# Kernel tuning notes

Hardware: AMD Instinct MI355X
Metric: run time of the kernel (lower is better)

## Reference

```python
import jax, jax.numpy as jnp
import numpy as np

H = 2048  # hidden_size == input_size
L = 2048  # max_length == seq_len


def setup_inputs() -> dict:
    key = jax.random.key(0)
    ks = jax.random.split(key, 5)
    bound = 1.0 / np.sqrt(H)  # torch nn.GRU default init: U(-1/sqrt(H), 1/sqrt(H))
    u = lambda k, shape: jax.random.uniform(k, shape, jnp.float32, -bound, bound)
    return {
        "x": jax.random.normal(ks[0], (L, H), jnp.float32),
        "w_ih": u(ks[1], (3 * H, H)),  # rows ordered [reset; update; new], torch layout
        "w_hh": u(ks[2], (3 * H, H)),
        "b_ih": u(ks[3], (3 * H,)),
        "b_hh": u(ks[4], (3 * H,)),
    }


def reference(x, w_ih, w_hh, b_ih, b_hh):
    # Faithful single-layer GRU (torch semantics), batch=1, hidden init to zeros.
    def step(h, x_t):
        gi = x_t @ w_ih.T + b_ih          # (3H,)
        gh = h @ w_hh.T + b_hh            # (3H,)
        i_r, i_z, i_n = jnp.split(gi, 3)
        h_r, h_z, h_n = jnp.split(gh, 3)
        r = jax.nn.sigmoid(i_r + h_r)
        z = jax.nn.sigmoid(i_z + h_z)
        n = jnp.tanh(i_n + r * h_n)
        h_new = (1.0 - z) * n + z * h
        return h_new, h_new

    h0 = jnp.zeros((H,), x.dtype)
    h_final, outputs = jax.lax.scan(step, h0, x)  # outputs: (L, H)
    hidden = h_final.reshape(1, 1, H)  # matches torch (num_layers, batch, H)
    return outputs, hidden, hidden
```

## Files before the change

kernel.cpp:

```cpp
#include <hip/hip_runtime.h>
#include <math.h>

#define HID 2048
#define SEQ 2048
#define N3  6144
#define NBLK 256
#define NREG 8

#define BM 128
#define BN 128
#define BK 16

__global__ __launch_bounds__(256)
void gi_gemm_kernel(const float* __restrict__ X, const float* __restrict__ W,
                    const float* __restrict__ bias, float* __restrict__ GI) {
  __shared__ float As[BK][BM + 4];
  __shared__ float Bs[BK][BN + 4];
  const int tid = threadIdx.x;
  const int bm = blockIdx.y * BM;
  const int bn = blockIdx.x * BN;
  const int tx = tid & 15;
  const int ty = tid >> 4;
  const int lr = tid >> 1;
  const int lk = (tid & 1) * 8;

  float acc[8][8];
#pragma unroll
  for (int i = 0; i < 8; ++i)
#pragma unroll
    for (int j = 0; j < 8; ++j) acc[i][j] = 0.f;

  const float* Arow = X + (size_t)(bm + lr) * HID + lk;
  const float* Brow = W + (size_t)(bn + lr) * HID + lk;

  for (int kc = 0; kc < HID; kc += BK) {
    float4 a0 = *(const float4*)(Arow + kc);
    float4 a1 = *(const float4*)(Arow + kc + 4);
    float4 b0 = *(const float4*)(Brow + kc);
    float4 b1 = *(const float4*)(Brow + kc + 4);
    __syncthreads();
    As[lk + 0][lr] = a0.x; As[lk + 1][lr] = a0.y; As[lk + 2][lr] = a0.z; As[lk + 3][lr] = a0.w;
    As[lk + 4][lr] = a1.x; As[lk + 5][lr] = a1.y; As[lk + 6][lr] = a1.z; As[lk + 7][lr] = a1.w;
    Bs[lk + 0][lr] = b0.x; Bs[lk + 1][lr] = b0.y; Bs[lk + 2][lr] = b0.z; Bs[lk + 3][lr] = b0.w;
    Bs[lk + 4][lr] = b1.x; Bs[lk + 5][lr] = b1.y; Bs[lk + 6][lr] = b1.z; Bs[lk + 7][lr] = b1.w;
    __syncthreads();
#pragma unroll
    for (int kk = 0; kk < BK; ++kk) {
      float4 av0 = *(const float4*)&As[kk][ty * 8];
      float4 av1 = *(const float4*)&As[kk][ty * 8 + 4];
      float4 bv0 = *(const float4*)&Bs[kk][tx * 8];
      float4 bv1 = *(const float4*)&Bs[kk][tx * 8 + 4];
      float a[8] = {av0.x, av0.y, av0.z, av0.w, av1.x, av1.y, av1.z, av1.w};
      float b[8] = {bv0.x, bv0.y, bv0.z, bv0.w, bv1.x, bv1.y, bv1.z, bv1.w};
#pragma unroll
      for (int i = 0; i < 8; ++i)
#pragma unroll
        for (int j = 0; j < 8; ++j)
          acc[i][j] = fmaf(a[i], b[j], acc[i][j]);
    }
  }

  const int n0 = bn + tx * 8;
  float bv[8];
#pragma unroll
  for (int j = 0; j < 8; ++j) bv[j] = bias[n0 + j];
#pragma unroll
  for (int i = 0; i < 8; ++i) {
    float4 o0, o1;
    o0.x = acc[i][0] + bv[0]; o0.y = acc[i][1] + bv[1];
    o0.z = acc[i][2] + bv[2]; o0.w = acc[i][3] + bv[3];
    o1.x = acc[i][4] + bv[4]; o1.y = acc[i][5] + bv[5];
    o1.z = acc[i][6] + bv[6]; o1.w = acc[i][7] + bv[7];
    float* Crow = GI + (size_t)(bm + ty * 8 + i) * N3 + n0;
    *(float4*)Crow = o0;
    *(float4*)(Crow + 4) = o1;
  }
}

template <int CTRL, int ROW_MASK>
__device__ __forceinline__ float dpp_add(float x) {
  int y = __builtin_amdgcn_update_dpp(0, __float_as_uint(x), CTRL, ROW_MASK, 0xf, true);
  return x + __uint_as_float(y);
}

__device__ __forceinline__ float wave_sum(float x) {
  x = dpp_add<0x111, 0xf>(x);
  x = dpp_add<0x112, 0xf>(x);
  x = dpp_add<0x114, 0xf>(x);
  x = dpp_add<0x118, 0xf>(x);
  x = dpp_add<0x142, 0xa>(x);
  x = dpp_add<0x143, 0xc>(x);
  return __uint_as_float(__builtin_amdgcn_readlane(__float_as_uint(x), 63));
}

__device__ __forceinline__ float rlane(float x, int l) {
  return __uint_as_float(__builtin_amdgcn_readlane(__float_as_uint(x), l));
}

__device__ __forceinline__ float sigf(float x) {
  return __builtin_amdgcn_rcpf(1.f + __expf(-x));
}
__device__ __forceinline__ float tanhfast(float x) {
  return 1.f - 2.f * __builtin_amdgcn_rcpf(1.f + __expf(2.f * x));
}

__device__ __forceinline__ float unpk24(unsigned u) {
  return __uint_as_float((u & 0x00FFFFFFu) << 8);
}

__device__ __forceinline__ void ld_quad2(const unsigned long long* pa,
                                         const unsigned long long* pb,
                                         uint4& qa, uint4& qb) {
  asm volatile("global_load_dwordx4 %0, %2, off sc1\n\t"
               "global_load_dwordx4 %1, %3, off sc1\n\t"
               "s_waitcnt vmcnt(0)"
               : "=&v"(qa), "=&v"(qb)
               : "v"(pa), "v"(pb)
               : "memory");
}

__global__ __launch_bounds__(256, 1)
void gru_recurrent_kernel(const float* __restrict__ Whh,
                          const float* __restrict__ bhh,
                          const float* __restrict__ GI,
                          float* __restrict__ out,
                          unsigned long long* hpk,
                          int t0, int t1) {
  __shared__ float lds_h[2][HID];
  const int tid  = threadIdx.x;
  const int lane = tid & 63;
  const int wv   = tid >> 6;
  const int gw   = blockIdx.x * 4 + wv;
  const int i0   = 2 * gw;
  const int reg  = blockIdx.x & (NREG - 1);

  const int rows[6] = {i0, i0 + 1, HID + i0, HID + i0 + 1, 2 * HID + i0, 2 * HID + i0 + 1};

  float4 w[6][8];
#pragma unroll
  for (int r = 0; r < 6; ++r) {
    const float* wr = Whh + (size_t)rows[r] * HID + lane * 4;
#pragma unroll
    for (int jb = 0; jb < 8; ++jb) {
      w[r][jb] = *(const float4*)(wr + jb * 256);
      asm volatile("" : "+a"(w[r][jb].x), "+a"(w[r][jb].y),
                        "+a"(w[r][jb].z), "+a"(w[r][jb].w));
    }
  }

  float br0, br1, bz0, bz1, bn0, bn1;
  {
    float a = 0.f, b = 0.f, c = 0.f;
    if (lane < 2) {
      a = bhh[i0 + lane];
      b = bhh[HID + i0 + lane];
      c = bhh[2 * HID + i0 + lane];
    }
    br0 = rlane(a, 0); br1 = rlane(a, 1);
    bz0 = rlane(b, 0); bz1 = rlane(b, 1);
    bn0 = rlane(c, 0); bn1 = rlane(c, 1);
  }

  float gr = 0.f, gz = 0.f, gn = 0.f;
  if (lane < 2) {
    gr = GI[i0 + lane];
    gz = GI[HID + i0 + lane];
    gn = GI[2 * HID + i0 + lane];
  }

  const int s0 = tid * 2;

  long long d_prev = 0;
  long long period = 0;
  const long long MARGIN = 1500;

  for (int t = t0; t < t1; ++t) {
    if (period > 0) {
      const long long target = d_prev + period - MARGIN;
      while ((long long)__builtin_amdgcn_s_memtime() < target)
        __builtin_amdgcn_s_sleep(1);
    }

    float pr = 0.f, pz = 0.f, pn = 0.f;
    if (t + 1 < t1 && lane < 2) {
      const float* g = GI + (size_t)(t + 1 - t0) * N3;
      pr = g[i0 + lane];
      pz = g[HID + i0 + lane];
      pn = g[2 * HID + i0 + lane];
    }
    asm volatile("" ::: "memory");

    const unsigned long long* hb = hpk + ((size_t)reg * 2 + (t & 1)) * (HID / 2);
    const unsigned long long* pa = hb + s0;
    const unsigned long long* pb = hb + 512 + s0;
    const unsigned tb = (unsigned)t & 0xFFu;
    uint4 qa, qb;
    ld_quad2(pa, pb, qa, qb);
    for (;;) {
      const bool ok = ((qa.x >> 24) == tb) & ((qa.y >> 24) == tb) &
                      ((qa.z >> 24) == tb) & ((qa.w >> 24) == tb) &
                      ((qb.x >> 24) == tb) & ((qb.y >> 24) == tb) &
                      ((qb.z >> 24) == tb) & ((qb.w >> 24) == tb);
      if (ok) break;
      ld_quad2(pa, pb, qa, qb);
    }

    {
      const long long now = (long long)__builtin_amdgcn_s_memtime();
      if (d_prev > 0) {
        const long long iv = now - d_prev;
        period = (period > 0) ? period + ((iv - period) >> 3) : iv;
        if (period > 20000) period = 20000;
        if (period < 0) period = 0;
      }
      d_prev = now;
    }

    float* lc = lds_h[t & 1];
    float4 v0, v1;
    v0.x = unpk24(qa.x); v0.y = unpk24(qa.y);
    v0.z = unpk24(qa.z); v0.w = unpk24(qa.w);
    v1.x = unpk24(qb.x); v1.y = unpk24(qb.y);
    v1.z = unpk24(qb.z); v1.w = unpk24(qb.w);
    *(float4*)&lc[tid * 4] = v0;
    *(float4*)&lc[1024 + tid * 4] = v1;
    __syncthreads();

    const float hp0 = lc[i0], hp1 = lc[i0 + 1];

    float4 hv[8];
    float acc0 = 0.f, acc1 = 0.f, acc2 = 0.f, acc3 = 0.f;
#pragma unroll
    for (int jb = 0; jb < 8; ++jb) {
      hv[jb] = *(const float4*)&lc[jb * 256 + lane * 4];
      acc0 = fmaf(w[0][jb].x, hv[jb].x, acc0); acc0 = fmaf(w[0][jb].y, hv[jb].y, acc0);
      acc0 = fmaf(w[0][jb].z, hv[jb].z, acc0); acc0 = fmaf(w[0][jb].w, hv[jb].w, acc0);
      acc1 = fmaf(w[1][jb].x, hv[jb].x, acc1); acc1 = fmaf(w[1][jb].y, hv[jb].y, acc1);
      acc1 = fmaf(w[1][jb].z, hv[jb].z, acc1); acc1 = fmaf(w[1][jb].w, hv[jb].w, acc1);
      acc2 = fmaf(w[2][jb].x, hv[jb].x, acc2); acc2 = fmaf(w[2][jb].y, hv[jb].y, acc2);
      acc2 = fmaf(w[2][jb].z, hv[jb].z, acc2); acc2 = fmaf(w[2][jb].w, hv[jb].w, acc2);
      acc3 = fmaf(w[3][jb].x, hv[jb].x, acc3); acc3 = fmaf(w[3][jb].y, hv[jb].y, acc3);
      acc3 = fmaf(w[3][jb].z, hv[jb].z, acc3); acc3 = fmaf(w[3][jb].w, hv[jb].w, acc3);
    }

    const float sr0 = wave_sum(acc0), sr1 = wave_sum(acc1);
    const float sz0 = wave_sum(acc2), sz1 = wave_sum(acc3);

    const float gr0 = rlane(gr, 0), gr1 = rlane(gr, 1);
    const float gz0 = rlane(gz, 0), gz1 = rlane(gz, 1);
    const float gn0 = rlane(gn, 0), gn1 = rlane(gn, 1);

    const float r0 = sigf(gr0 + sr0 + br0);
    const float r1 = sigf(gr1 + sr1 + br1);
    const float z0 = sigf(gz0 + sz0 + bz0);
    const float z1 = sigf(gz1 + sz1 + bz1);

    float acc4 = 0.f, acc5 = 0.f;
#pragma unroll
    for (int jb = 0; jb < 8; ++jb) {
      acc4 = fmaf(w[4][jb].x, hv[jb].x, acc4); acc4 = fmaf(w[4][jb].y, hv[jb].y, acc4);
      acc4 = fmaf(w[4][jb].z, hv[jb].z, acc4); acc4 = fmaf(w[4][jb].w, hv[jb].w, acc4);
      acc5 = fmaf(w[5][jb].x, hv[jb].x, acc5); acc5 = fmaf(w[5][jb].y, hv[jb].y, acc5);
      acc5 = fmaf(w[5][jb].z, hv[jb].z, acc5); acc5 = fmaf(w[5][jb].w, hv[jb].w, acc5);
    }
    const float sn0 = wave_sum(acc4), sn1 = wave_sum(acc5);

    const float n0 = tanhfast(gn0 + r0 * (sn0 + bn0));
    const float n1 = tanhfast(gn1 + r1 * (sn1 + bn1));
    const float hn0 = (1.f - z0) * n0 + z0 * hp0;
    const float hn1 = (1.f - z1) * n1 + z1 * hp1;

    {
      const unsigned nt = ((unsigned)(t + 1) & 0xFFu) << 24;
      const unsigned u0 = (__float_as_uint(hn0) + 0x80u) >> 8;
      const unsigned u1 = (__float_as_uint(hn1) + 0x80u) >> 8;
      const unsigned long long pk =
          ((unsigned long long)(nt | (u1 & 0x00FFFFFFu)) << 32) |
          (nt | (u0 & 0x00FFFFFFu));
      if (lane < NREG) {
        __hip_atomic_store(hpk + ((size_t)lane * 2 + ((t + 1) & 1)) * (HID / 2) + gw,
                           pk, __ATOMIC_RELAXED, __HIP_MEMORY_SCOPE_AGENT);
      }
    }

    if (t > 0 && (t & (NBLK - 1)) == blockIdx.x) {
      float* orow = out + (size_t)(t - 1) * HID;
      *(float4*)(orow + tid * 4) = v0;
      *(float4*)(orow + 1024 + tid * 4) = v1;
    }

    if (t == SEQ - 1 && lane == 0) {
      float2 hv2; hv2.x = hn0; hv2.y = hn1;
      *(float2*)(out + (size_t)t * HID + i0) = hv2;
      *(float2*)(out + (size_t)SEQ * HID + i0) = hv2;
      *(float2*)(out + (size_t)SEQ * HID + HID + i0) = hv2;
    }

    gr = pr; gz = pz; gn = pn;
  }
}

extern "C" void kernel_launch(void* const* d_in, const int* in_sizes, int n_in,
                              void* d_out, int out_size, void* d_ws, size_t ws_size,
                              hipStream_t stream) {
  const float* x    = (const float*)d_in[0];
  const float* w_ih = (const float*)d_in[1];
  const float* w_hh = (const float*)d_in[2];
  const float* b_ih = (const float*)d_in[3];
  const float* b_hh = (const float*)d_in[4];
  float* out = (float*)d_out;

  const size_t hpk_bytes = (size_t)NREG * 2 * (HID / 2) * 8;

  int chunk = SEQ;
  while (chunk > 128 &&
         (size_t)chunk * N3 * 4 + hpk_bytes + 256 > ws_size)
    chunk >>= 1;

  const size_t gi_bytes = (size_t)chunk * N3 * 4;
  float* gi = (float*)d_ws;
  unsigned long long* hpk = (unsigned long long*)((char*)d_ws + gi_bytes);

  (void)hipMemsetAsync(hpk, 0, hpk_bytes, stream);

  for (int t0 = 0; t0 < SEQ; t0 += chunk) {
    dim3 ggrid(N3 / BN, chunk / BM);
    gi_gemm_kernel<<<ggrid, 256, 0, stream>>>(x + (size_t)t0 * HID, w_ih, b_ih, gi);
    gru_recurrent_kernel<<<NBLK, 256, 0, stream>>>(w_hh, b_hh, gi, out, hpk,
                                                   t0, t0 + chunk);
  }
}
```

Measured before the change: 4.922 ms.

## Compute input-gate GEMM with split-bf16 MFMA instead of FP32 FMA

Adds a kernel that splits x and w_ih into hi/lo bf16 pairs. It replaces the FP32 SIMT GEMM for the input projections with a bf16 MFMA GEMM that accumulates three cross products (hi*hi, hi*lo, lo*hi), giving near-FP32 accuracy on matrix cores. The aim is to cut the time of the non-recurrent GEMM. The cost is two extra conversion passes and more workspace, and the new GEMM loads operands straight from global memory with no LDS staging. The old path remains as a fallback when workspace is too small.

```diff
diff --git a/kernel.cpp b/kernel.cpp
--- a/kernel.cpp
+++ b/kernel.cpp
@@ -6,6 +6,9 @@
 #define N3  6144
 #define NBLK 256
 #define NREG 8
+
+typedef short bhalf8 __attribute__((ext_vector_type(8)));
+typedef float f32x4v __attribute__((ext_vector_type(4)));
 
 #define BM 128
 #define BN 128
@@ -74,6 +77,94 @@
     float* Crow = GI + (size_t)(bm + ty * 8 + i) * N3 + n0;
     *(float4*)Crow = o0;
     *(float4*)(Crow + 4) = o1;
+  }
+}
+
+__global__ __launch_bounds__(256)
+void split_bf16_kernel(const float* __restrict__ src,
+                       unsigned short* __restrict__ hi,
+                       unsigned short* __restrict__ lo, int n4) {
+  const int i = blockIdx.x * 256 + threadIdx.x;
+  if (i >= n4) return;
+  float4 v = *(const float4*)(src + (size_t)i * 4);
+  ushort4 h, l;
+#define SP(c, hc, lc)                                                \
+  {                                                                  \
+    unsigned u = __float_as_uint(v.c);                               \
+    unsigned hb = (u + 0x7FFFu + ((u >> 16) & 1u)) >> 16;            \
+    float lf = v.c - __uint_as_float(hb << 16);                      \
+    unsigned ul = __float_as_uint(lf);                               \
+    unsigned lb = (ul + 0x7FFFu + ((ul >> 16) & 1u)) >> 16;          \
+    hc = (unsigned short)hb; lc = (unsigned short)lb;                \
+  }
+  SP(x, h.x, l.x) SP(y, h.y, l.y) SP(z, h.z, l.z) SP(w, h.w, l.w)
+#undef SP
+  *(ushort4*)(hi + (size_t)i * 4) = h;
+  *(ushort4*)(lo + (size_t)i * 4) = l;
+}
+
+__global__ __launch_bounds__(256)
+void gi_gemm_mfma(const unsigned short* __restrict__ Xhi,
+                  const unsigned short* __restrict__ Xlo,
+                  const unsigned short* __restrict__ Whi,
+                  const unsigned short* __restrict__ Wlo,
+                  const float* __restrict__ bias, float* __restrict__ GI) {
+  const int lane = threadIdx.x & 63;
+  const int wv   = threadIdx.x >> 6;
+  const int wm = wv >> 1, wn = wv & 1;
+  const int m0 = blockIdx.y * 64 + wm * 32;
+  const int n0 = blockIdx.x * 128 + wn * 64;
+  const int lr = lane & 15;
+  const int lk = (lane >> 4) * 8;
+
+  f32x4v acc[2][4];
+#pragma unroll
+  for (int i = 0; i < 2; ++i)
+#pragma unroll
+    for (int j = 0; j < 4; ++j) {
+      f32x4v z = {0.f, 0.f, 0.f, 0.f};
+      acc[i][j] = z;
+    }
+
+  const unsigned short* xh = Xhi + (size_t)(m0 + lr) * HID + lk;
+  const unsigned short* xl = Xlo + (size_t)(m0 + lr) * HID + lk;
+  const unsigned short* wh = Whi + (size_t)(n0 + lr) * HID + lk;
+  const unsigned short* wl = Wlo + (size_t)(n0 + lr) * HID + lk;
+
+  for (int k0 = 0; k0 < HID; k0 += 32) {
+    bhalf8 ah0 = *(const bhalf8*)(xh + k0);
+    bhalf8 ah1 = *(const bhalf8*)(xh + (size_t)16 * HID + k0);
+    bhalf8 al0 = *(const bhalf8*)(xl + k0);
+    bhalf8 al1 = *(const bhalf8*)(xl + (size_t)16 * HID + k0);
+    bhalf8 bh[4], bl[4];
+#pragma unroll
+    for (int j = 0; j < 4; ++j) {
+      bh[j] = *(const bhalf8*)(wh + (size_t)j * 16 * HID + k0);
+      bl[j] = *(const bhalf8*)(wl + (size_t)j * 16 * HID + k0);
+    }
+#pragma unroll
+    for (int j = 0; j < 4; ++j) {
+      acc[0][j] = __builtin_amdgcn_mfma_f32_16x16x32_bf16(ah0, bh[j], acc[0][j], 0, 0, 0);
+      acc[0][j] = __builtin_amdgcn_mfma_f32_16x16x32_bf16(ah0, bl[j], acc[0][j], 0, 0, 0);
+      acc[0][j] = __builtin_amdgcn_mfma_f32_16x16x32_bf16(al0, bh[j], acc[0][j], 0, 0, 0);
+      acc[1][j] = __builtin_amdgcn_mfma_f32_16x16x32_bf16(ah1, bh[j], acc[1][j], 0, 0, 0);
+      acc[1][j] = __builtin_amdgcn_mfma_f32_16x16x32_bf16(ah1, bl[j], acc[1][j], 0, 0, 0);
+      acc[1][j] = __builtin_amdgcn_mfma_f32_16x16x32_bf16(al1, bh[j], acc[1][j], 0, 0, 0);
+    }
+  }
+
+  const int r0 = (lane >> 4) * 4;
+#pragma unroll
+  for (int j = 0; j < 4; ++j) {
+    const int col = n0 + j * 16 + lr;
+    const float bv = bias[col];
+#pragma unroll
+    for (int mi = 0; mi < 2; ++mi) {
+#pragma unroll
+      for (int r = 0; r < 4; ++r) {
+        GI[(size_t)(m0 + mi * 16 + r0 + r) * N3 + col] = acc[mi][j][r] + bv;
+      }
+    }
   }
 }
 
@@ -311,22 +402,56 @@
   float* out = (float*)d_out;
 
   const size_t hpk_bytes = (size_t)NREG * 2 * (HID / 2) * 8;
+  const size_t xs  = (size_t)SEQ * HID * sizeof(unsigned short);
+  const size_t wsp = (size_t)N3 * HID * sizeof(unsigned short);
 
   int chunk = SEQ;
   while (chunk > 128 &&
-         (size_t)chunk * N3 * 4 + hpk_bytes + 256 > ws_size)
+         (size_t)chunk * N3 * 4 + hpk_bytes + 2 * xs + 2 * wsp + 1024 > ws_size)
     chunk >>= 1;
-
-  const size_t gi_bytes = (size_t)chunk * N3 * 4;
-  float* gi = (float*)d_ws;
-  unsigned long long* hpk = (unsigned long long*)((char*)d_ws + gi_bytes);
-
-  (void)hipMemsetAsync(hpk, 0, hpk_bytes, stream);
-
-  for (int t0 = 0; t0 < SEQ; t0 += chunk) {
-    dim3 ggrid(N3 / BN, chunk / BM);
-    gi_gemm_kernel<<<ggrid, 256, 0, stream>>>(x + (size_t)t0 * HID, w_ih, b_ih, gi);
-    gru_recurrent_kernel<<<NBLK, 256, 0, stream>>>(w_hh, b_hh, gi, out, hpk,
-                                                   t0, t0 + chunk);
-  }
-}
+  const bool use_mfma =
+      ((size_t)chunk * N3 * 4 + hpk_bytes + 2 * xs + 2 * wsp + 1024 <= ws_size);
+
+  if (use_mfma) {
+    char* p = (char*)d_ws;
+    float* gi = (float*)p;                    p += (size_t)chunk * N3 * 4;
+    unsigned long long* hpk = (unsigned long long*)p;  p += hpk_bytes;
+    unsigned short* Xhi = (unsigned short*)p; p += xs;
+    unsigned short* Xlo = (unsigned short*)p; p += xs;
+    unsigned short* Whi = (unsigned short*)p; p += wsp;
+    unsigned short* Wlo = (unsigned short*)p;
+
+    (void)hipMemsetAsync(hpk, 0, hpk_bytes, stream);
+    split_bf16_kernel<<<(SEQ * HID / 4 + 255) / 256, 256, 0, stream>>>(
+        x, Xhi, Xlo, SEQ * HID / 4);
+    split_bf16_kernel<<<(N3 * HID / 4 + 255) / 256, 256, 0, stream>>>(
+        w_ih, Whi, Wlo, N3 * HID / 4);
+
+    for (int t0 = 0; t0 < SEQ; t0 += chunk) {
+      dim3 g(N3 / 128, chunk / 64);
+      gi_gemm_mfma<<<g, 256, 0, stream>>>(Xhi + (size_t)t0 * HID,
+                                          Xlo + (size_t)t0 * HID,
+                                          Whi, Wlo, b_ih, gi);
+      gru_recurrent_kernel<<<NBLK, 256, 0, stream>>>(w_hh, b_hh, gi, out, hpk,
+                                                     t0, t0 + chunk);
+    }
+  } else {
+    int fchunk = SEQ;
+    while (fchunk > 128 &&
+           (size_t)fchunk * N3 * 4 + hpk_bytes + 256 > ws_size)
+      fchunk >>= 1;
+
+    const size_t gi_bytes = (size_t)fchunk * N3 * 4;
+    float* gi = (float*)d_ws;
+    unsigned long long* hpk = (unsigned long long*)((char*)d_ws + gi_bytes);
+
+    (void)hipMemsetAsync(hpk, 0, hpk_bytes, stream);
+
+    for (int t0 = 0; t0 < SEQ; t0 += fchunk) {
+      dim3 ggrid(N3 / BN, fchunk / BM);
+      gi_gemm_kernel<<<ggrid, 256, 0, stream>>>(x + (size_t)t0 * HID, w_ih, b_ih, gi);
+      gru_recurrent_kernel<<<NBLK, 256, 0, stream>>>(w_hh, b_hh, gi, out, hpk,
+                                                     t0, t0 + fchunk);
+    }
+  }
+}
```

Result: no change. 4.853 ms (-1.4%).
